# Optimization experiments

Measured on AMD Instinct MI355X. Metric: run time of the kernel, lower is better.

## Reference

```python
import jax, jax.numpy as jnp
import numpy as np

EMBED_DIM = 128
NUM_HEADS = 4
WINDOW = 7
N = WINDOW * WINDOW
HEAD_DIM = EMBED_DIM // NUM_HEADS


def _relative_position_index(w):
    ch, cw = np.meshgrid(np.arange(w), np.arange(w), indexing='ij')
    coords = np.stack([ch, cw]).reshape(2, -1)            # [2, N]
    rel = coords[:, :, None] - coords[:, None, :]          # [2, N, N]
    rel = rel.transpose(1, 2, 0)                           # [N, N, 2]
    rel[:, :, 0] += w - 1
    rel[:, :, 1] += w - 1
    rel[:, :, 0] *= 2 * w - 1
    return rel.sum(-1)                                     # [N, N]


def setup_inputs() -> dict:
    key = jax.random.key(0)
    ks = jax.random.split(key, 6)
    B_ = 8192
    C = EMBED_DIM
    std = 0.02
    x = jax.random.normal(ks[0], (B_, N, C), dtype=jnp.float32)
    qkv_w = jax.random.normal(ks[1], (3 * C, C), dtype=jnp.float32) * (C ** -0.5)
    qkv_b = jnp.zeros((3 * C,), dtype=jnp.float32)
    out_w = jax.random.normal(ks[2], (C, C), dtype=jnp.float32) * (C ** -0.5)
    out_b = jnp.zeros((C,), dtype=jnp.float32)
    bias_table = jax.random.normal(ks[3], ((2 * WINDOW - 1) ** 2, NUM_HEADS), dtype=jnp.float32) * std
    rel_idx = jnp.asarray(_relative_position_index(WINDOW), dtype=jnp.int32)  # [N, N]
    return {"x": x, "qkv_w": qkv_w, "qkv_b": qkv_b, "out_w": out_w,
            "out_b": out_b, "bias_table": bias_table, "rel_idx": rel_idx}


def reference(x, qkv_w, qkv_b, out_w, out_b, bias_table, rel_idx):
    B_, n, C = x.shape
    H, D = NUM_HEADS, HEAD_DIM
    qkv = x @ qkv_w.T + qkv_b                               # [B, N, 3C]
    qkv = qkv.reshape(B_, n, 3, H, D).transpose(2, 0, 3, 1, 4)
    q, k, v = qkv[0], qkv[1], qkv[2]                        # each [B, H, N, D]
    scale = D ** -0.5
    attn = jnp.einsum('bhnd,bhmd->bhnm', q, k) * scale      # [B, H, N, N]
    bias = bias_table[rel_idx]                              # [N, N, H]
    attn = attn + bias.transpose(2, 0, 1)[None]             # broadcast over B
    attn = jax.nn.softmax(attn.astype(jnp.float32), axis=-1).astype(x.dtype)
    out = jnp.einsum('bhnm,bhmd->bhnd', attn, v)            # [B, H, N, D]
    out = out.transpose(0, 2, 1, 3).reshape(B_, n, C)
    return out @ out_w.T + out_b
```

## Files before the change

### kernel.cpp

```cpp
#include <hip/hip_runtime.h>

#define NWIN   8192
#define NTOK   49
#define CDIM   128
#define NHEAD  4
#define HDIM   32

typedef __attribute__((ext_vector_type(8))) short bf16x8;
typedef __attribute__((ext_vector_type(4))) float f32x4;

#define MFMA __builtin_amdgcn_mfma_f32_16x16x32_bf16

__device__ __forceinline__ unsigned short f2bf(float f) {
  union { float f; unsigned int u; } v; v.f = f;
  unsigned int r = v.u + 0x7FFFu + ((v.u >> 16) & 1u);
  return (unsigned short)(r >> 16);
}

__device__ __forceinline__ int cvtpk(float lo, float hi) {
  int r;
  asm("v_cvt_pk_bf16_f32 %0, %1, %2" : "=v"(r) : "v"(lo), "v"(hi));
  return r;
}

__global__ void swin_prep(const float* __restrict__ qkv_w,
                          const float* __restrict__ out_w,
                          const float* __restrict__ bias_table,
                          const int* __restrict__ rel_idx,
                          unsigned short* __restrict__ wqkv,
                          unsigned short* __restrict__ wout,
                          float* __restrict__ biasf) {
  int idx = blockIdx.x * 256 + threadIdx.x;
  if (idx < 3 * CDIM * CDIM) {
    float v = qkv_w[idx];
    if (idx < CDIM * CDIM) v *= 0.17677669529663687f;
    wqkv[idx] = f2bf(v);
  }
  if (idx < CDIM * CDIM) wout[idx] = f2bf(out_w[idx]);
  if (idx < NHEAD * 4 * 4 * 64 * 4) {
    int r    = idx & 3;
    int lane = (idx >> 2) & 63;
    int j    = (idx >> 8) & 3;
    int i    = (idx >> 10) & 3;
    int h    = (idx >> 12);
    int n = i * 16 + (lane & 15);
    int m = j * 16 + (lane >> 4) * 4 + r;
    float v = 0.f;
    if (n < NTOK && m < NTOK)
      v = bias_table[rel_idx[n * NTOK + m] * NHEAD + h];
    biasf[idx] = v;
  }
}

__global__ __launch_bounds__(256, 1) void swin_fused(
    const float* __restrict__ x,
    const unsigned short* __restrict__ wqkv,
    const float* __restrict__ bqkv,
    const unsigned short* __restrict__ wout,
    const float* __restrict__ bout,
    const float* __restrict__ biasf,
    float* __restrict__ out)
{
  const int lane = threadIdx.x & 63;
  const int l15  = lane & 15;
  const int lg   = lane >> 4;
  const int win  = blockIdx.x * 4 + (threadIdx.x >> 6);

  const int srcA = l15 + 32 * (lg & 1);
  const int srcB = srcA + 16;
  const bool sel = ((lg >> 1) & 1) != 0;

  const f32x4 fz = {0.f, 0.f, 0.f, 0.f};

  #define XCHG(res, E0, E1, O0, O1)                                   \
    {                                                                  \
      int a0 = __shfl((E0), srcA, 64), b0 = __shfl((O0), srcA, 64);    \
      int a1 = __shfl((E1), srcA, 64), b1 = __shfl((O1), srcA, 64);    \
      int a2 = __shfl((E0), srcB, 64), b2 = __shfl((O0), srcB, 64);    \
      int a3 = __shfl((E1), srcB, 64), b3 = __shfl((O1), srcB, 64);    \
      union { int w[4]; bf16x8 v; } ux;                                \
      ux.w[0] = sel ? b0 : a0;                                         \
      ux.w[1] = sel ? b1 : a1;                                         \
      ux.w[2] = sel ? b2 : a2;                                         \
      ux.w[3] = sel ? b3 : a3;                                         \
      res = ux.v;                                                      \
    }

  bf16x8 xa[4][4];
  const float* xw = x + (size_t)win * (NTOK * CDIM);
  #pragma unroll
  for (int i = 0; i < 4; ++i) {
    int row = i * 16 + l15; row = row > 48 ? 48 : row;
    const float* xr = xw + row * CDIM + lg * 8;
    #pragma unroll
    for (int kk = 0; kk < 4; ++kk) {
      float4 a = *reinterpret_cast<const float4*>(xr + kk * 32);
      float4 b = *reinterpret_cast<const float4*>(xr + kk * 32 + 4);
      union { int w[4]; bf16x8 v; } t;
      t.w[0] = cvtpk(a.x, a.y); t.w[1] = cvtpk(a.z, a.w);
      t.w[2] = cvtpk(b.x, b.y); t.w[3] = cvtpk(b.z, b.w);
      xa[i][kk] = t.v;
    }
  }

  bf16x8 af[4][4];

  #pragma unroll
  for (int h = 0; h < NHEAD; ++h) {
    int dwV[2][4][2];
    #pragma unroll
    for (int t = 0; t < 2; ++t) {
      const unsigned short* wr = wqkv + (size_t)(2 * CDIM + h * HDIM + t * 16 + l15) * CDIM + lg * 8;
      bf16x8 wb[4];
      #pragma unroll
      for (int kk = 0; kk < 4; ++kk) wb[kk] = *reinterpret_cast<const bf16x8*>(wr + kk * 32);
      const float bv = bqkv[2 * CDIM + h * HDIM + t * 16 + l15];
      #pragma unroll
      for (int i = 0; i < 4; ++i) {
        f32x4 acc = fz;
        #pragma unroll
        for (int kk = 0; kk < 4; ++kk) acc = MFMA(xa[i][kk], wb[kk], acc, 0, 0, 0);
        dwV[t][i][0] = cvtpk(acc[0] + bv, acc[1] + bv);
        dwV[t][i][1] = cvtpk(acc[2] + bv, acc[3] + bv);
      }
    }
    bf16x8 vf[2][2];
    #pragma unroll
    for (int t = 0; t < 2; ++t)
      #pragma unroll
      for (int kk2 = 0; kk2 < 2; ++kk2)
        XCHG(vf[t][kk2], dwV[t][kk2 * 2][0], dwV[t][kk2 * 2][1],
                          dwV[t][kk2 * 2 + 1][0], dwV[t][kk2 * 2 + 1][1]);

    bf16x8 qf[4], kf[4];
    #pragma unroll
    for (int s = 0; s < 2; ++s) {
      int dwQ[2][4][2];
      #pragma unroll
      for (int t = 0; t < 2; ++t) {
        const int colbase = s * CDIM + h * HDIM + t * 16;
        const unsigned short* wr = wqkv + (size_t)(colbase + l15) * CDIM + lg * 8;
        bf16x8 wb[4];
        #pragma unroll
        for (int kk = 0; kk < 4; ++kk) wb[kk] = *reinterpret_cast<const bf16x8*>(wr + kk * 32);
        float4 b4 = *reinterpret_cast<const float4*>(bqkv + colbase + lg * 4);
        if (s == 0) { b4.x *= 0.17677669529663687f; b4.y *= 0.17677669529663687f;
                      b4.z *= 0.17677669529663687f; b4.w *= 0.17677669529663687f; }
        #pragma unroll
        for (int i = 0; i < 4; ++i) {
          f32x4 acc = fz;
          #pragma unroll
          for (int kk = 0; kk < 4; ++kk) acc = MFMA(wb[kk], xa[i][kk], acc, 0, 0, 0);
          dwQ[t][i][0] = cvtpk(acc[0] + b4.x, acc[1] + b4.y);
          dwQ[t][i][1] = cvtpk(acc[2] + b4.z, acc[3] + b4.w);
        }
      }
      #pragma unroll
      for (int i = 0; i < 4; ++i) {
        bf16x8 f;
        XCHG(f, dwQ[0][i][0], dwQ[0][i][1], dwQ[1][i][0], dwQ[1][i][1]);
        if (s == 0) qf[i] = f; else kf[i] = f;
      }
    }

    #pragma unroll
    for (int i = 0; i < 4; ++i) {
      f32x4 sj[4];
      #pragma unroll
      for (int j = 0; j < 4; ++j) sj[j] = MFMA(kf[j], qf[i], fz, 0, 0, 0);
      #pragma unroll
      for (int j = 0; j < 4; ++j) {
        float4 bb = *reinterpret_cast<const float4*>(
            biasf + ((((h * 4 + i) * 4 + j) * 64 + lane) * 4));
        sj[j][0] += bb.x; sj[j][1] += bb.y; sj[j][2] += bb.z; sj[j][3] += bb.w;
      }
      sj[3][0] = (lg == 0) ? sj[3][0] : -1e30f;
      sj[3][1] = -1e30f; sj[3][2] = -1e30f; sj[3][3] = -1e30f;

      float mx = sj[0][0];
      #pragma unroll
      for (int j = 0; j < 4; ++j)
        #pragma unroll
        for (int r = 0; r < 4; ++r) mx = fmaxf(mx, sj[j][r]);
      mx = fmaxf(mx, __shfl_xor(mx, 16, 64));
      mx = fmaxf(mx, __shfl_xor(mx, 32, 64));
      float sm = 0.f;
      #pragma unroll
      for (int j = 0; j < 4; ++j)
        #pragma unroll
        for (int r = 0; r < 4; ++r) {
          float p = __expf(sj[j][r] - mx);
          sj[j][r] = p; sm += p;
        }
      sm += __shfl_xor(sm, 16, 64);
      sm += __shfl_xor(sm, 32, 64);
      const float inv = 1.f / sm;

      int dwP[4][2];
      #pragma unroll
      for (int j = 0; j < 4; ++j) {
        dwP[j][0] = cvtpk(sj[j][0] * inv, sj[j][1] * inv);
        dwP[j][1] = cvtpk(sj[j][2] * inv, sj[j][3] * inv);
      }
      bf16x8 pa0, pa1;
      XCHG(pa0, dwP[0][0], dwP[0][1], dwP[1][0], dwP[1][1]);
      XCHG(pa1, dwP[2][0], dwP[2][1], dwP[3][0], dwP[3][1]);

      f32x4 o0 = MFMA(vf[0][0], pa0, fz, 0, 0, 0);
      o0 = MFMA(vf[0][1], pa1, o0, 0, 0, 0);
      f32x4 o1 = MFMA(vf[1][0], pa0, fz, 0, 0, 0);
      o1 = MFMA(vf[1][1], pa1, o1, 0, 0, 0);

      int a00 = cvtpk(o0[0], o0[1]), a01 = cvtpk(o0[2], o0[3]);
      int a10 = cvtpk(o1[0], o1[1]), a11 = cvtpk(o1[2], o1[3]);
      XCHG(af[h][i], a00, a01, a10, a11);
    }
  }

  float* ow = out + (size_t)win * (NTOK * CDIM);
  #pragma unroll
  for (int j = 0; j < 8; ++j) {
    bf16x8 wb2[4];
    #pragma unroll
    for (int h = 0; h < 4; ++h)
      wb2[h] = *reinterpret_cast<const bf16x8*>(wout + (size_t)(j * 16 + l15) * CDIM + h * HDIM + lg * 8);
    f32x4 acc[4];
    #pragma unroll
    for (int i = 0; i < 4; ++i) acc[i] = fz;
    #pragma unroll
    for (int h = 0; h < 4; ++h)
      #pragma unroll
      for (int i = 0; i < 4; ++i)
        acc[i] = MFMA(af[h][i], wb2[h], acc[i], 0, 0, 0);
    const float ob = bout[j * 16 + l15];
    #pragma unroll
    for (int i = 0; i < 4; ++i)
      #pragma unroll
      for (int r = 0; r < 4; ++r) {
        int n = i * 16 + lg * 4 + r;
        if (n < NTOK) ow[n * CDIM + j * 16 + l15] = acc[i][r] + ob;
      }
  }
  #undef XCHG
}

extern "C" void kernel_launch(void* const* d_in, const int* in_sizes, int n_in,
                              void* d_out, int out_size, void* d_ws, size_t ws_size,
                              hipStream_t stream) {
  (void)in_sizes; (void)n_in; (void)out_size; (void)ws_size;
  const float* x          = (const float*)d_in[0];
  const float* qkv_w      = (const float*)d_in[1];
  const float* qkv_b      = (const float*)d_in[2];
  const float* out_w      = (const float*)d_in[3];
  const float* out_b      = (const float*)d_in[4];
  const float* bias_table = (const float*)d_in[5];
  const int*   rel_idx    = (const int*)d_in[6];
  float* out = (float*)d_out;

  unsigned short* wqkv = (unsigned short*)d_ws;
  unsigned short* wout = wqkv + 3 * CDIM * CDIM;
  float* biasf = (float*)((char*)d_ws + 131072);

  swin_prep<<<192, 256, 0, stream>>>(qkv_w, out_w, bias_table, rel_idx, wqkv, wout, biasf);
  swin_fused<<<NWIN / 4, 256, 0, stream>>>(x, wqkv, qkv_b, wout, out_b, biasf, out);
}
```

Before: 216.2 us.

## Split heads across wavefronts, one window per block, via LDS exchange

Each block now handles a single window, with each of its four wavefronts computing one attention head instead of one wave looping over all heads. Per-head outputs are staged in shared memory, and after a barrier each wave computes two column tiles of the output projection. Dropping the min-blocks launch bound and the large per-thread af array lowers register pressure, which should allow higher occupancy and more parallelism. The cost is that every wave still loads and converts the full x tile, so global reads of x grow fourfold (likely from cache), plus LDS traffic and a block barrier.

```diff
diff --git a/kernel.cpp b/kernel.cpp
--- a/kernel.cpp
+++ b/kernel.cpp
@@ -52,7 +52,7 @@
   }
 }
 
-__global__ __launch_bounds__(256, 1) void swin_fused(
+__global__ __launch_bounds__(256) void swin_fused(
     const float* __restrict__ x,
     const unsigned short* __restrict__ wqkv,
     const float* __restrict__ bqkv,
@@ -61,10 +61,13 @@
     const float* __restrict__ biasf,
     float* __restrict__ out)
 {
+  __shared__ unsigned short ao[64 * 136];
+
   const int lane = threadIdx.x & 63;
   const int l15  = lane & 15;
   const int lg   = lane >> 4;
-  const int win  = blockIdx.x * 4 + (threadIdx.x >> 6);
+  const int h    = threadIdx.x >> 6;
+  const int win  = blockIdx.x;
 
   const int srcA = l15 + 32 * (lg & 1);
   const int srcB = srcA + 16;
@@ -103,135 +106,138 @@
     }
   }
 
-  bf16x8 af[4][4];
-
-  #pragma unroll
-  for (int h = 0; h < NHEAD; ++h) {
-    int dwV[2][4][2];
+  int dwV[2][4][2];
+  #pragma unroll
+  for (int t = 0; t < 2; ++t) {
+    const unsigned short* wr = wqkv + (size_t)(2 * CDIM + h * HDIM + t * 16 + l15) * CDIM + lg * 8;
+    bf16x8 wb[4];
+    #pragma unroll
+    for (int kk = 0; kk < 4; ++kk) wb[kk] = *reinterpret_cast<const bf16x8*>(wr + kk * 32);
+    const float bv = bqkv[2 * CDIM + h * HDIM + t * 16 + l15];
+    #pragma unroll
+    for (int i = 0; i < 4; ++i) {
+      f32x4 acc = fz;
+      #pragma unroll
+      for (int kk = 0; kk < 4; ++kk) acc = MFMA(xa[i][kk], wb[kk], acc, 0, 0, 0);
+      dwV[t][i][0] = cvtpk(acc[0] + bv, acc[1] + bv);
+      dwV[t][i][1] = cvtpk(acc[2] + bv, acc[3] + bv);
+    }
+  }
+  bf16x8 vf[2][2];
+  #pragma unroll
+  for (int t = 0; t < 2; ++t)
+    #pragma unroll
+    for (int kk2 = 0; kk2 < 2; ++kk2)
+      XCHG(vf[t][kk2], dwV[t][kk2 * 2][0], dwV[t][kk2 * 2][1],
+                        dwV[t][kk2 * 2 + 1][0], dwV[t][kk2 * 2 + 1][1]);
+
+  bf16x8 qf[4], kf[4];
+  #pragma unroll
+  for (int s = 0; s < 2; ++s) {
+    int dwQ[2][4][2];
     #pragma unroll
     for (int t = 0; t < 2; ++t) {
-      const unsigned short* wr = wqkv + (size_t)(2 * CDIM + h * HDIM + t * 16 + l15) * CDIM + lg * 8;
+      const int colbase = s * CDIM + h * HDIM + t * 16;
+      const unsigned short* wr = wqkv + (size_t)(colbase + l15) * CDIM + lg * 8;
       bf16x8 wb[4];
       #pragma unroll
       for (int kk = 0; kk < 4; ++kk) wb[kk] = *reinterpret_cast<const bf16x8*>(wr + kk * 32);
-      const float bv = bqkv[2 * CDIM + h * HDIM + t * 16 + l15];
+      float4 b4 = *reinterpret_cast<const float4*>(bqkv + colbase + lg * 4);
+      if (s == 0) { b4.x *= 0.17677669529663687f; b4.y *= 0.17677669529663687f;
+                    b4.z *= 0.17677669529663687f; b4.w *= 0.17677669529663687f; }
       #pragma unroll
       for (int i = 0; i < 4; ++i) {
         f32x4 acc = fz;
         #pragma unroll
-        for (int kk = 0; kk < 4; ++kk) acc = MFMA(xa[i][kk], wb[kk], acc, 0, 0, 0);
-        dwV[t][i][0] = cvtpk(acc[0] + bv, acc[1] + bv);
-        dwV[t][i][1] = cvtpk(acc[2] + bv, acc[3] + bv);
-      }
-    }
-    bf16x8 vf[2][2];
-    #pragma unroll
-    for (int t = 0; t < 2; ++t)
-      #pragma unroll
-      for (int kk2 = 0; kk2 < 2; ++kk2)
-        XCHG(vf[t][kk2], dwV[t][kk2 * 2][0], dwV[t][kk2 * 2][1],
-                          dwV[t][kk2 * 2 + 1][0], dwV[t][kk2 * 2 + 1][1]);
-
-    bf16x8 qf[4], kf[4];
-    #pragma unroll
-    for (int s = 0; s < 2; ++s) {
-      int dwQ[2][4][2];
-      #pragma unroll
-      for (int t = 0; t < 2; ++t) {
-        const int colbase = s * CDIM + h * HDIM + t * 16;
-        const unsigned short* wr = wqkv + (size_t)(colbase + l15) * CDIM + lg * 8;
-        bf16x8 wb[4];
-        #pragma unroll
-        for (int kk = 0; kk < 4; ++kk) wb[kk] = *reinterpret_cast<const bf16x8*>(wr + kk * 32);
-        float4 b4 = *reinterpret_cast<const float4*>(bqkv + colbase + lg * 4);
-        if (s == 0) { b4.x *= 0.17677669529663687f; b4.y *= 0.17677669529663687f;
-                      b4.z *= 0.17677669529663687f; b4.w *= 0.17677669529663687f; }
-        #pragma unroll
-        for (int i = 0; i < 4; ++i) {
-          f32x4 acc = fz;
-          #pragma unroll
-          for (int kk = 0; kk < 4; ++kk) acc = MFMA(wb[kk], xa[i][kk], acc, 0, 0, 0);
-          dwQ[t][i][0] = cvtpk(acc[0] + b4.x, acc[1] + b4.y);
-          dwQ[t][i][1] = cvtpk(acc[2] + b4.z, acc[3] + b4.w);
-        }
-      }
+        for (int kk = 0; kk < 4; ++kk) acc = MFMA(wb[kk], xa[i][kk], acc, 0, 0, 0);
+        dwQ[t][i][0] = cvtpk(acc[0] + b4.x, acc[1] + b4.y);
+        dwQ[t][i][1] = cvtpk(acc[2] + b4.z, acc[3] + b4.w);
+      }
+    }
+    #pragma unroll
+    for (int i = 0; i < 4; ++i) {
+      bf16x8 f;
+      XCHG(f, dwQ[0][i][0], dwQ[0][i][1], dwQ[1][i][0], dwQ[1][i][1]);
+      if (s == 0) qf[i] = f; else kf[i] = f;
+    }
+  }
+
+  #pragma unroll
+  for (int i = 0; i < 4; ++i) {
+    f32x4 sj[4];
+    #pragma unroll
+    for (int j = 0; j < 4; ++j) sj[j] = MFMA(kf[j], qf[i], fz, 0, 0, 0);
+    #pragma unroll
+    for (int j = 0; j < 4; ++j) {
+      float4 bb = *reinterpret_cast<const float4*>(
+          biasf + ((((h * 4 + i) * 4 + j) * 64 + lane) * 4));
+      sj[j][0] += bb.x; sj[j][1] += bb.y; sj[j][2] += bb.z; sj[j][3] += bb.w;
+    }
+    sj[3][0] = (lg == 0) ? sj[3][0] : -1e30f;
+    sj[3][1] = -1e30f; sj[3][2] = -1e30f; sj[3][3] = -1e30f;
+
+    float mx = sj[0][0];
+    #pragma unroll
+    for (int j = 0; j < 4; ++j)
+      #pragma unroll
+      for (int r = 0; r < 4; ++r) mx = fmaxf(mx, sj[j][r]);
+    mx = fmaxf(mx, __shfl_xor(mx, 16, 64));
+    mx = fmaxf(mx, __shfl_xor(mx, 32, 64));
+    float sm = 0.f;
+    #pragma unroll
+    for (int j = 0; j < 4; ++j)
+      #pragma unroll
+      for (int r = 0; r < 4; ++r) {
+        float p = __expf(sj[j][r] - mx);
+        sj[j][r] = p; sm += p;
+      }
+    sm += __shfl_xor(sm, 16, 64);
+    sm += __shfl_xor(sm, 32, 64);
+    const float inv = 1.f / sm;
+
+    int dwP[4][2];
+    #pragma unroll
+    for (int j = 0; j < 4; ++j) {
+      dwP[j][0] = cvtpk(sj[j][0] * inv, sj[j][1] * inv);
+      dwP[j][1] = cvtpk(sj[j][2] * inv, sj[j][3] * inv);
+    }
+    bf16x8 pa0, pa1;
+    XCHG(pa0, dwP[0][0], dwP[0][1], dwP[1][0], dwP[1][1]);
+    XCHG(pa1, dwP[2][0], dwP[2][1], dwP[3][0], dwP[3][1]);
+
+    f32x4 o0 = MFMA(vf[0][0], pa0, fz, 0, 0, 0);
+    o0 = MFMA(vf[0][1], pa1, o0, 0, 0, 0);
+    f32x4 o1 = MFMA(vf[1][0], pa0, fz, 0, 0, 0);
+    o1 = MFMA(vf[1][1], pa1, o1, 0, 0, 0);
+
+    union { int w[2]; long long ll; } p0, p1;
+    p0.w[0] = cvtpk(o0[0], o0[1]); p0.w[1] = cvtpk(o0[2], o0[3]);
+    p1.w[0] = cvtpk(o1[0], o1[1]); p1.w[1] = cvtpk(o1[2], o1[3]);
+    unsigned short* base = &ao[(i * 16 + l15) * 136 + h * HDIM];
+    *reinterpret_cast<long long*>(base + lg * 4)      = p0.ll;
+    *reinterpret_cast<long long*>(base + 16 + lg * 4) = p1.ll;
+  }
+
+  __syncthreads();
+
+  float* ow = out + (size_t)win * (NTOK * CDIM);
+  #pragma unroll
+  for (int jj = 0; jj < 2; ++jj) {
+    const int j = h * 2 + jj;
+    f32x4 acc[4];
+    #pragma unroll
+    for (int i = 0; i < 4; ++i) acc[i] = fz;
+    #pragma unroll
+    for (int h2 = 0; h2 < 4; ++h2) {
+      bf16x8 wb2 = *reinterpret_cast<const bf16x8*>(
+          wout + (size_t)(j * 16 + l15) * CDIM + h2 * HDIM + lg * 8);
       #pragma unroll
       for (int i = 0; i < 4; ++i) {
-        bf16x8 f;
-        XCHG(f, dwQ[0][i][0], dwQ[0][i][1], dwQ[1][i][0], dwQ[1][i][1]);
-        if (s == 0) qf[i] = f; else kf[i] = f;
-      }
-    }
-
-    #pragma unroll
-    for (int i = 0; i < 4; ++i) {
-      f32x4 sj[4];
-      #pragma unroll
-      for (int j = 0; j < 4; ++j) sj[j] = MFMA(kf[j], qf[i], fz, 0, 0, 0);
-      #pragma unroll
-      for (int j = 0; j < 4; ++j) {
-        float4 bb = *reinterpret_cast<const float4*>(
-            biasf + ((((h * 4 + i) * 4 + j) * 64 + lane) * 4));
-        sj[j][0] += bb.x; sj[j][1] += bb.y; sj[j][2] += bb.z; sj[j][3] += bb.w;
-      }
-      sj[3][0] = (lg == 0) ? sj[3][0] : -1e30f;
-      sj[3][1] = -1e30f; sj[3][2] = -1e30f; sj[3][3] = -1e30f;
-
-      float mx = sj[0][0];
-      #pragma unroll
-      for (int j = 0; j < 4; ++j)
-        #pragma unroll
-        for (int r = 0; r < 4; ++r) mx = fmaxf(mx, sj[j][r]);
-      mx = fmaxf(mx, __shfl_xor(mx, 16, 64));
-      mx = fmaxf(mx, __shfl_xor(mx, 32, 64));
-      float sm = 0.f;
-      #pragma unroll
-      for (int j = 0; j < 4; ++j)
-        #pragma unroll
-        for (int r = 0; r < 4; ++r) {
-          float p = __expf(sj[j][r] - mx);
-          sj[j][r] = p; sm += p;
-        }
-      sm += __shfl_xor(sm, 16, 64);
-      sm += __shfl_xor(sm, 32, 64);
-      const float inv = 1.f / sm;
-
-      int dwP[4][2];
-      #pragma unroll
-      for (int j = 0; j < 4; ++j) {
-        dwP[j][0] = cvtpk(sj[j][0] * inv, sj[j][1] * inv);
-        dwP[j][1] = cvtpk(sj[j][2] * inv, sj[j][3] * inv);
-      }
-      bf16x8 pa0, pa1;
-      XCHG(pa0, dwP[0][0], dwP[0][1], dwP[1][0], dwP[1][1]);
-      XCHG(pa1, dwP[2][0], dwP[2][1], dwP[3][0], dwP[3][1]);
-
-      f32x4 o0 = MFMA(vf[0][0], pa0, fz, 0, 0, 0);
-      o0 = MFMA(vf[0][1], pa1, o0, 0, 0, 0);
-      f32x4 o1 = MFMA(vf[1][0], pa0, fz, 0, 0, 0);
-      o1 = MFMA(vf[1][1], pa1, o1, 0, 0, 0);
-
-      int a00 = cvtpk(o0[0], o0[1]), a01 = cvtpk(o0[2], o0[3]);
-      int a10 = cvtpk(o1[0], o1[1]), a11 = cvtpk(o1[2], o1[3]);
-      XCHG(af[h][i], a00, a01, a10, a11);
-    }
-  }
-
-  float* ow = out + (size_t)win * (NTOK * CDIM);
-  #pragma unroll
-  for (int j = 0; j < 8; ++j) {
-    bf16x8 wb2[4];
-    #pragma unroll
-    for (int h = 0; h < 4; ++h)
-      wb2[h] = *reinterpret_cast<const bf16x8*>(wout + (size_t)(j * 16 + l15) * CDIM + h * HDIM + lg * 8);
-    f32x4 acc[4];
-    #pragma unroll
-    for (int i = 0; i < 4; ++i) acc[i] = fz;
-    #pragma unroll
-    for (int h = 0; h < 4; ++h)
-      #pragma unroll
-      for (int i = 0; i < 4; ++i)
-        acc[i] = MFMA(af[h][i], wb2[h], acc[i], 0, 0, 0);
+        bf16x8 ab = *reinterpret_cast<const bf16x8*>(
+            &ao[(i * 16 + l15) * 136 + h2 * HDIM + lg * 8]);
+        acc[i] = MFMA(ab, wb2, acc[i], 0, 0, 0);
+      }
+    }
     const float ob = bout[j * 16 + l15];
     #pragma unroll
     for (int i = 0; i < 4; ++i)
@@ -262,5 +268,5 @@
   float* biasf = (float*)((char*)d_ws + 131072);
 
   swin_prep<<<192, 256, 0, stream>>>(qkv_w, out_w, bias_table, rel_idx, wqkv, wout, biasf);
-  swin_fused<<<NWIN / 4, 256, 0, stream>>>(x, wqkv, qkv_b, wout, out_b, biasf, out);
-}
+  swin_fused<<<NWIN, 256, 0, stream>>>(x, wqkv, qkv_b, wout, out_b, biasf, out);
+}
```

New measurement: 333.2 us. +54.1%, slower.
